# Kernel optimization log

Hardware: AMD Instinct MI355X
Metric: run time of the kernel (lower is better)

## Reference

```python
import jax, jax.numpy as jnp
import numpy as np

N_USERS = 100_000
N_ITEMS = 50_000
N = N_USERS + N_ITEMS
N_LAYERS = 3
ALPHA = 0.8
D = 64
IMG_D = 4096
TXT_D = 384
N_INTER = 2_000_000  # user-item interactions; symmetric nnz = 2*N_INTER


def setup_inputs() -> dict:
    # --- build symmetric-normalized bipartite adjacency (D^-1/2 A D^-1/2) in numpy ---
    rng = np.random.default_rng(0)
    u = rng.integers(0, N_USERS, N_INTER).astype(np.int32)
    i = (rng.integers(0, N_ITEMS, N_INTER) + N_USERS).astype(np.int32)
    rows = np.concatenate([u, i])
    cols = np.concatenate([i, u])
    deg = np.bincount(rows, minlength=N).astype(np.float32)
    d_inv = np.where(deg > 0, deg ** -0.5, 0.0).astype(np.float32)
    vals = d_inv[rows] * d_inv[cols]

    key = jax.random.key(0)
    ks = jax.random.split(key, 8)
    xav_img = float(np.sqrt(6.0 / (IMG_D + D)))
    xav_txt = float(np.sqrt(6.0 / (TXT_D + D)))
    return {
        "image_feats": jax.random.normal(ks[0], (N_ITEMS, IMG_D), jnp.float32),
        "text_feats": jax.random.normal(ks[1], (N_ITEMS, TXT_D), jnp.float32),
        "image_pref": jax.random.normal(ks[2], (N_USERS, D), jnp.float32),
        "text_pref": jax.random.normal(ks[3], (N_USERS, D), jnp.float32),
        "W_img": jax.random.uniform(ks[4], (IMG_D, D), jnp.float32, -xav_img, xav_img),
        "b_img": jnp.zeros((D,), jnp.float32),
        "W_txt": jax.random.uniform(ks[5], (TXT_D, D), jnp.float32, -xav_txt, xav_txt),
        "b_txt": jnp.zeros((D,), jnp.float32),
        "adj_vals": jnp.asarray(vals),
        "adj_rows": jnp.asarray(rows),
        "adj_cols": jnp.asarray(cols),
    }


def _spmm(rows, cols, vals, x):
    # sparse COO @ dense: out[r] += vals[e] * x[cols[e]]
    return jax.ops.segment_sum(vals[:, None] * x[cols], rows, num_segments=N)


def _l2norm(x):
    # F.normalize(x, dim=1): row-wise L2 with eps clamp
    return x / jnp.clip(jnp.linalg.norm(x, axis=1, keepdims=True), 1e-12)


def reference(image_feats, text_feats, image_pref, text_pref,
              W_img, b_img, W_txt, b_txt, adj_vals, adj_rows, adj_cols):
    img = _l2norm(image_feats @ W_img + b_img)   # [n_items, D]
    txt = _l2norm(text_feats @ W_txt + b_txt)    # [n_items, D]
    ego_i = jnp.concatenate([image_pref, img], axis=0)  # [N, D]
    ego_t = jnp.concatenate([text_pref, txt], axis=0)   # [N, D]
    for _ in range(N_LAYERS):
        ego_i = _spmm(adj_rows, adj_cols, adj_vals, ego_i) + ALPHA * ego_i
        ego_t = _spmm(adj_rows, adj_cols, adj_vals, ego_t) + ALPHA * ego_t
    user_preference = jnp.concatenate([ego_i[:N_USERS], ego_t[:N_USERS]], axis=1)  # [n_users, 2D]
    items = jnp.concatenate([ego_i[N_USERS:], ego_t[N_USERS:]], axis=1)            # [n_items, 2D]
    return user_preference, items
```

## Files before the change

### kernel.cpp

```cpp
#include <hip/hip_runtime.h>
#include <hip/hip_bf16.h>

#define N_USERS 100000
#define N_ITEMS 50000
#define N_TOTAL 150000
#define NNZ     4000000
#define ALPHA_F 0.8f
#define ELL_CAP 128

#define G_GEMM 782
#define G_COPY 512
#define G_SCAT 1024

typedef __attribute__((ext_vector_type(8))) short bf16x8;
typedef __attribute__((ext_vector_type(4))) float f32x4;

static __device__ __forceinline__ short f2bf(float f) {
    unsigned u = __builtin_bit_cast(unsigned, f);
    unsigned r = (u + 0x7fff + ((u >> 16) & 1)) >> 16;
    return (short)r;
}
static __device__ __forceinline__ unsigned pack_bf2(float a, float b) {
    return (unsigned)(unsigned short)f2bf(a) | ((unsigned)(unsigned short)f2bf(b) << 16);
}
static __device__ __forceinline__ float bf_lo(unsigned u) { return __uint_as_float(u << 16); }
static __device__ __forceinline__ float bf_hi(unsigned u) { return __uint_as_float(u & 0xFFFF0000u); }


__global__ __launch_bounds__(256) void prep_kernel(const float* __restrict__ Wimg,
                                                   const float* __restrict__ Wtxt,
                                                   int* __restrict__ cnt,
                                                   short* __restrict__ Wti,
                                                   short* __restrict__ Wtt) {
    const int T0 = N_TOTAL;
    const int T1 = T0 + 4096 * 64;
    const int T2 = T1 + 384 * 64;
    int i = blockIdx.x * 256 + threadIdx.x;
    int stride = gridDim.x * 256;
    for (; i < T2; i += stride) {
        if (i < T0) {
            cnt[i] = 0;
        } else if (i < T1) {
            int idx = i - T0; int k = idx >> 6, n = idx & 63;
            Wti[(size_t)n * 4096 + k] = f2bf(Wimg[(size_t)k * 64 + n]);
        } else {
            int idx = i - T1; int k = idx >> 6, n = idx & 63;
            Wtt[(size_t)n * 384 + k] = f2bf(Wtxt[(size_t)k * 64 + n]);
        }
    }
}


__global__ __launch_bounds__(256) void mega_kernel(
        const float* __restrict__ Aimg, const float* __restrict__ Atxt,
        const short* __restrict__ Wti, const short* __restrict__ Wtt,
        const float* __restrict__ bimg, const float* __restrict__ btxt,
        unsigned* __restrict__ egob,
        const int* __restrict__ rows, const int* __restrict__ cols,
        const float* __restrict__ vals, int* __restrict__ cnt, int2* __restrict__ ell,
        const float* __restrict__ img_pref, const float* __restrict__ txt_pref) {
    int b = blockIdx.x;
    if (b < G_GEMM) {
        const int M = N_ITEMS;
        int t = threadIdx.x;
        int wave = t >> 6, l = t & 63;
        int col = l & 15;
        int kb  = l >> 4;
        int row0 = b * 64 + wave * 16;
        int arow = row0 + col;
        bool rowok = arow < M;

        f32x4 ai0 = {0,0,0,0}, ai1 = ai0, ai2 = ai0, ai3 = ai0;
        f32x4 at0 = ai0, at1 = ai0, at2 = ai0, at3 = ai0;

        {
            const float* Ap = Aimg + (size_t)arow * 4096 + kb * 8;
            const short* Wp = Wti + (size_t)col * 4096 + kb * 8;
            for (int k0 = 0; k0 < 4096; k0 += 32) {
                float4 a0 = make_float4(0,0,0,0), a1 = a0;
                if (rowok) {
                    a0 = *reinterpret_cast<const float4*>(Ap + k0);
                    a1 = *reinterpret_cast<const float4*>(Ap + k0 + 4);
                }
                bf16x8 af;
                af[0]=f2bf(a0.x); af[1]=f2bf(a0.y); af[2]=f2bf(a0.z); af[3]=f2bf(a0.w);
                af[4]=f2bf(a1.x); af[5]=f2bf(a1.y); af[6]=f2bf(a1.z); af[7]=f2bf(a1.w);
                bf16x8 b0 = *reinterpret_cast<const bf16x8*>(Wp + k0);
                bf16x8 b1 = *reinterpret_cast<const bf16x8*>(Wp + (size_t)16 * 4096 + k0);
                bf16x8 b2 = *reinterpret_cast<const bf16x8*>(Wp + (size_t)32 * 4096 + k0);
                bf16x8 b3 = *reinterpret_cast<const bf16x8*>(Wp + (size_t)48 * 4096 + k0);
                ai0 = __builtin_amdgcn_mfma_f32_16x16x32_bf16(af, b0, ai0, 0, 0, 0);
                ai1 = __builtin_amdgcn_mfma_f32_16x16x32_bf16(af, b1, ai1, 0, 0, 0);
                ai2 = __builtin_amdgcn_mfma_f32_16x16x32_bf16(af, b2, ai2, 0, 0, 0);
                ai3 = __builtin_amdgcn_mfma_f32_16x16x32_bf16(af, b3, ai3, 0, 0, 0);
            }
        }
        {
            const float* Ap = Atxt + (size_t)arow * 384 + kb * 8;
            const short* Wp = Wtt + (size_t)col * 384 + kb * 8;
            for (int k0 = 0; k0 < 384; k0 += 32) {
                float4 a0 = make_float4(0,0,0,0), a1 = a0;
                if (rowok) {
                    a0 = *reinterpret_cast<const float4*>(Ap + k0);
                    a1 = *reinterpret_cast<const float4*>(Ap + k0 + 4);
                }
                bf16x8 af;
                af[0]=f2bf(a0.x); af[1]=f2bf(a0.y); af[2]=f2bf(a0.z); af[3]=f2bf(a0.w);
                af[4]=f2bf(a1.x); af[5]=f2bf(a1.y); af[6]=f2bf(a1.z); af[7]=f2bf(a1.w);
                bf16x8 b0 = *reinterpret_cast<const bf16x8*>(Wp + k0);
                bf16x8 b1 = *reinterpret_cast<const bf16x8*>(Wp + (size_t)16 * 384 + k0);
                bf16x8 b2 = *reinterpret_cast<const bf16x8*>(Wp + (size_t)32 * 384 + k0);
                bf16x8 b3 = *reinterpret_cast<const bf16x8*>(Wp + (size_t)48 * 384 + k0);
                at0 = __builtin_amdgcn_mfma_f32_16x16x32_bf16(af, b0, at0, 0, 0, 0);
                at1 = __builtin_amdgcn_mfma_f32_16x16x32_bf16(af, b1, at1, 0, 0, 0);
                at2 = __builtin_amdgcn_mfma_f32_16x16x32_bf16(af, b2, at2, 0, 0, 0);
                at3 = __builtin_amdgcn_mfma_f32_16x16x32_bf16(af, b3, at3, 0, 0, 0);
            }
        }

        float bi0 = bimg[ 0 + col], bi1 = bimg[16 + col], bi2 = bimg[32 + col], bi3 = bimg[48 + col];
        float bt0 = btxt[ 0 + col], bt1 = btxt[16 + col], bt2 = btxt[32 + col], bt3 = btxt[48 + col];
        #pragma unroll
        for (int i = 0; i < 4; ++i) {
            ai0[i] += bi0; ai1[i] += bi1; ai2[i] += bi2; ai3[i] += bi3;
            at0[i] += bt0; at1[i] += bt1; at2[i] += bt2; at3[i] += bt3;
        }
        unsigned* egob_items = egob + (size_t)N_USERS * 64;
        #pragma unroll
        for (int i = 0; i < 4; ++i) {
            float ssi = ai0[i]*ai0[i] + ai1[i]*ai1[i] + ai2[i]*ai2[i] + ai3[i]*ai3[i];
            float sst = at0[i]*at0[i] + at1[i]*at1[i] + at2[i]*at2[i] + at3[i]*at3[i];
            #pragma unroll
            for (int off = 1; off < 16; off <<= 1) {
                ssi += __shfl_xor(ssi, off, 64);
                sst += __shfl_xor(sst, off, 64);
            }
            float rni = 1.0f / fmaxf(sqrtf(ssi), 1e-12f);
            float rnt = 1.0f / fmaxf(sqrtf(sst), 1e-12f);
            int r = row0 + kb * 4 + i;
            if (r < M) {
                unsigned* ob = egob_items + (size_t)r * 64 + col;
                ob[ 0] = pack_bf2(ai0[i]*rni, at0[i]*rnt);
                ob[16] = pack_bf2(ai1[i]*rni, at1[i]*rnt);
                ob[32] = pack_bf2(ai2[i]*rni, at2[i]*rnt);
                ob[48] = pack_bf2(ai3[i]*rni, at3[i]*rnt);
            }
        }
    } else if (b < G_GEMM + G_COPY) {
        int idx = (b - G_GEMM) * 256 + threadIdx.x;
        int stride = G_COPY * 256;
        for (; idx < N_USERS * 16; idx += stride) {
            int row = idx >> 4, w4 = (idx & 15) << 2;
            float4 iv = *reinterpret_cast<const float4*>(&img_pref[(size_t)row * 64 + w4]);
            float4 tv = *reinterpret_cast<const float4*>(&txt_pref[(size_t)row * 64 + w4]);
            uint4 m;
            m.x = pack_bf2(iv.x, tv.x); m.y = pack_bf2(iv.y, tv.y);
            m.z = pack_bf2(iv.z, tv.z); m.w = pack_bf2(iv.w, tv.w);
            *reinterpret_cast<uint4*>(&egob[(size_t)row * 64 + w4]) = m;
        }
    } else {
        int i = (b - G_GEMM - G_COPY) * 256 + threadIdx.x;
        int stride = G_SCAT * 256;
        for (; i < NNZ; i += stride) {
            int r = rows[i];
            int p = atomicAdd(&cnt[r], 1);
            if (p < ELL_CAP)
                ell[(size_t)r * ELL_CAP + p] = make_int2(cols[i], __float_as_int(vals[i]));
        }
    }
}


__global__ __launch_bounds__(256) void sort_kernel(const int* __restrict__ cnt,
                                                   int2* __restrict__ ell) {
    int row = blockIdx.x * 4 + (threadIdx.x >> 6);
    if (row >= N_TOTAL) return;
    int lane = threadIdx.x & 63;
    int deg = min(cnt[row], ELL_CAP);
    if (deg <= 1) return;
    int2* base = ell + (size_t)row * ELL_CAP;
    int2 e0 = (lane < deg)      ? base[lane]      : make_int2(0x7FFFFFFF, 0);
    int2 e1 = (lane + 64 < deg) ? base[lane + 64] : make_int2(0x7FFFFFFF, 0);
    #pragma unroll
    for (int k = 2; k <= 128; k <<= 1) {
        #pragma unroll
        for (int j = 64; j >= 1; j >>= 1) {
            if (j >= k) continue;
            if (j == 64) {
                if (e0.x > e1.x) { int2 tmp = e0; e0 = e1; e1 = tmp; }
            } else {
                int2 p0, p1;
                p0.x = __shfl_xor(e0.x, j, 64); p0.y = __shfl_xor(e0.y, j, 64);
                p1.x = __shfl_xor(e1.x, j, 64); p1.y = __shfl_xor(e1.y, j, 64);
                bool up0 = ((lane & k) == 0);
                bool up1 = (((lane + 64) & k) == 0);
                bool lo0 = ((lane & j) == 0);
                bool lo1 = lo0;
                bool keepmin0 = (up0 == lo0);
                bool keepmin1 = (up1 == lo1);
                if (keepmin0 ? (e0.x > p0.x) : (e0.x < p0.x)) e0 = p0;
                if (keepmin1 ? (e1.x > p1.x) : (e1.x < p1.x)) e1 = p1;
            }
        }
    }
    if (lane < deg)      base[lane]      = e0;
    if (lane + 64 < deg) base[lane + 64] = e1;
}


__global__ __launch_bounds__(256) void spmm_kernel(
        const int* __restrict__ cnt, const int2* __restrict__ ell,
        const unsigned* __restrict__ xb,
        float* __restrict__ out32, unsigned* __restrict__ outb) {
    int row = blockIdx.x * 4 + (threadIdx.x >> 6);
    if (row >= N_TOTAL) return;
    int lane = threadIdx.x & 63;
    unsigned sw = xb[(size_t)row * 64 + lane];
    float2 acc;
    acc.x = ALPHA_F * bf_lo(sw);
    acc.y = ALPHA_F * bf_hi(sw);
    int deg = min(cnt[row], ELL_CAP);
    const int2* base = ell + (size_t)row * ELL_CAP;
    int i = 0;
    for (; i + 8 <= deg; i += 8) {
        int4 p0 = *reinterpret_cast<const int4*>(base + i);
        int4 p1 = *reinterpret_cast<const int4*>(base + i + 2);
        int4 p2 = *reinterpret_cast<const int4*>(base + i + 4);
        int4 p3 = *reinterpret_cast<const int4*>(base + i + 6);
        unsigned g0 = xb[(size_t)p0.x * 64 + lane];
        unsigned g1 = xb[(size_t)p0.z * 64 + lane];
        unsigned g2 = xb[(size_t)p1.x * 64 + lane];
        unsigned g3 = xb[(size_t)p1.z * 64 + lane];
        unsigned g4 = xb[(size_t)p2.x * 64 + lane];
        unsigned g5 = xb[(size_t)p2.z * 64 + lane];
        unsigned g6 = xb[(size_t)p3.x * 64 + lane];
        unsigned g7 = xb[(size_t)p3.z * 64 + lane];
        float v0 = __int_as_float(p0.y), v1 = __int_as_float(p0.w);
        float v2 = __int_as_float(p1.y), v3 = __int_as_float(p1.w);
        float v4 = __int_as_float(p2.y), v5 = __int_as_float(p2.w);
        float v6 = __int_as_float(p3.y), v7 = __int_as_float(p3.w);
        acc.x = fmaf(v0, bf_lo(g0), acc.x); acc.y = fmaf(v0, bf_hi(g0), acc.y);
        acc.x = fmaf(v1, bf_lo(g1), acc.x); acc.y = fmaf(v1, bf_hi(g1), acc.y);
        acc.x = fmaf(v2, bf_lo(g2), acc.x); acc.y = fmaf(v2, bf_hi(g2), acc.y);
        acc.x = fmaf(v3, bf_lo(g3), acc.x); acc.y = fmaf(v3, bf_hi(g3), acc.y);
        acc.x = fmaf(v4, bf_lo(g4), acc.x); acc.y = fmaf(v4, bf_hi(g4), acc.y);
        acc.x = fmaf(v5, bf_lo(g5), acc.x); acc.y = fmaf(v5, bf_hi(g5), acc.y);
        acc.x = fmaf(v6, bf_lo(g6), acc.x); acc.y = fmaf(v6, bf_hi(g6), acc.y);
        acc.x = fmaf(v7, bf_lo(g7), acc.x); acc.y = fmaf(v7, bf_hi(g7), acc.y);
    }
    for (; i < deg; ++i) {
        int2 c = base[i];
        float v = __int_as_float(c.y);
        unsigned g = xb[(size_t)c.x * 64 + lane];
        acc.x = fmaf(v, bf_lo(g), acc.x);
        acc.y = fmaf(v, bf_hi(g), acc.y);
    }
    if (out32) {
        out32[(size_t)row * 128 + lane] = acc.x;
        out32[(size_t)row * 128 + 64 + lane] = acc.y;
    }
    if (outb)
        outb[(size_t)row * 64 + lane] = pack_bf2(acc.x, acc.y);
}


extern "C" void kernel_launch(void* const* d_in, const int* in_sizes, int n_in,
                              void* d_out, int out_size, void* d_ws, size_t ws_size,
                              hipStream_t stream) {
    const float* image_feats = (const float*)d_in[0];
    const float* text_feats  = (const float*)d_in[1];
    const float* image_pref  = (const float*)d_in[2];
    const float* text_pref   = (const float*)d_in[3];
    const float* W_img       = (const float*)d_in[4];
    const float* b_img       = (const float*)d_in[5];
    const float* W_txt       = (const float*)d_in[6];
    const float* b_txt       = (const float*)d_in[7];
    const float* adj_vals    = (const float*)d_in[8];
    const int*   adj_rows    = (const int*)d_in[9];
    const int*   adj_cols    = (const int*)d_in[10];

    float* out = (float*)d_out;

    char* ws = (char*)d_ws;
    size_t off = 0;
    auto alloc = [&](size_t bytes) { char* p = ws + off; off += (bytes + 255) & ~size_t(255); return p; };
    int*      cnt    = (int*)     alloc(N_TOTAL * sizeof(int));
    int2*     ell    = (int2*)    alloc((size_t)N_TOTAL * ELL_CAP * sizeof(int2));
    unsigned* m0     = (unsigned*)alloc((size_t)N_TOTAL * 64 * sizeof(unsigned));
    unsigned* m1     = (unsigned*)alloc((size_t)N_TOTAL * 64 * sizeof(unsigned));
    short*    Wt_img = (short*)   alloc((size_t)64 * 4096 * sizeof(short));
    short*    Wt_txt = (short*)   alloc((size_t)64 * 384 * sizeof(short));
    (void)ws_size; (void)out_size; (void)n_in; (void)in_sizes;

    prep_kernel<<<512, 256, 0, stream>>>(W_img, W_txt, cnt, Wt_img, Wt_txt);

    mega_kernel<<<G_GEMM + G_COPY + G_SCAT, 256, 0, stream>>>(
        image_feats, text_feats, Wt_img, Wt_txt, b_img, b_txt, m0,
        adj_rows, adj_cols, adj_vals, cnt, ell, image_pref, text_pref);

    const int ROW_GRID = (N_TOTAL + 3) / 4;
    sort_kernel<<<ROW_GRID, 256, 0, stream>>>(cnt, ell);

    spmm_kernel<<<ROW_GRID, 256, 0, stream>>>(cnt, ell, m0, nullptr, m1);
    spmm_kernel<<<ROW_GRID, 256, 0, stream>>>(cnt, ell, m1, nullptr, m0);
    spmm_kernel<<<ROW_GRID, 256, 0, stream>>>(cnt, ell, m0, out, nullptr);
}
```

Measured before the change: 1.181 ms.

## Split GEMM into LDS double-buffered kernel with direct global-to-LDS loads

Moves the item projection GEMM out of the fused mega kernel into its own kernel. The new kernel stages A and W tiles into swizzled, double-buffered LDS with global_load_lds, so the next chunk loads while MFMA runs on the current one. This replaces the per-lane strided global loads of the old version. The scatter/copy work now runs as a separate kernel before the GEMM instead of concurrently in the same grid, which costs some overlap and adds a launch.

```diff
diff --git a/kernel.cpp b/kernel.cpp
--- a/kernel.cpp
+++ b/kernel.cpp
@@ -7,10 +7,10 @@
 #define NNZ     4000000
 #define ALPHA_F 0.8f
 #define ELL_CAP 128
-
-#define G_GEMM 782
-#define G_COPY 512
-#define G_SCAT 1024
+#define KCHUNK  128
+
+#define C_COPY 512
+#define C_SCAT 1024
 
 typedef __attribute__((ext_vector_type(8))) short bf16x8;
 typedef __attribute__((ext_vector_type(4))) float f32x4;
@@ -25,6 +25,12 @@
 }
 static __device__ __forceinline__ float bf_lo(unsigned u) { return __uint_as_float(u << 16); }
 static __device__ __forceinline__ float bf_hi(unsigned u) { return __uint_as_float(u & 0xFFFF0000u); }
+
+static __device__ __forceinline__ void gload_lds16(const void* src, void* dst) {
+    __builtin_amdgcn_global_load_lds(
+        (const __attribute__((address_space(1))) unsigned*)src,
+        (__attribute__((address_space(3))) unsigned*)dst, 16, 0, 0);
+}
 
 
 __global__ __launch_bounds__(256) void prep_kernel(const float* __restrict__ Wimg,
@@ -51,104 +57,15 @@
 }
 
 
-__global__ __launch_bounds__(256) void mega_kernel(
-        const float* __restrict__ Aimg, const float* __restrict__ Atxt,
-        const short* __restrict__ Wti, const short* __restrict__ Wtt,
-        const float* __restrict__ bimg, const float* __restrict__ btxt,
-        unsigned* __restrict__ egob,
+__global__ __launch_bounds__(256) void scat_copy_kernel(
         const int* __restrict__ rows, const int* __restrict__ cols,
         const float* __restrict__ vals, int* __restrict__ cnt, int2* __restrict__ ell,
-        const float* __restrict__ img_pref, const float* __restrict__ txt_pref) {
+        const float* __restrict__ img_pref, const float* __restrict__ txt_pref,
+        unsigned* __restrict__ egob) {
     int b = blockIdx.x;
-    if (b < G_GEMM) {
-        const int M = N_ITEMS;
-        int t = threadIdx.x;
-        int wave = t >> 6, l = t & 63;
-        int col = l & 15;
-        int kb  = l >> 4;
-        int row0 = b * 64 + wave * 16;
-        int arow = row0 + col;
-        bool rowok = arow < M;
-
-        f32x4 ai0 = {0,0,0,0}, ai1 = ai0, ai2 = ai0, ai3 = ai0;
-        f32x4 at0 = ai0, at1 = ai0, at2 = ai0, at3 = ai0;
-
-        {
-            const float* Ap = Aimg + (size_t)arow * 4096 + kb * 8;
-            const short* Wp = Wti + (size_t)col * 4096 + kb * 8;
-            for (int k0 = 0; k0 < 4096; k0 += 32) {
-                float4 a0 = make_float4(0,0,0,0), a1 = a0;
-                if (rowok) {
-                    a0 = *reinterpret_cast<const float4*>(Ap + k0);
-                    a1 = *reinterpret_cast<const float4*>(Ap + k0 + 4);
-                }
-                bf16x8 af;
-                af[0]=f2bf(a0.x); af[1]=f2bf(a0.y); af[2]=f2bf(a0.z); af[3]=f2bf(a0.w);
-                af[4]=f2bf(a1.x); af[5]=f2bf(a1.y); af[6]=f2bf(a1.z); af[7]=f2bf(a1.w);
-                bf16x8 b0 = *reinterpret_cast<const bf16x8*>(Wp + k0);
-                bf16x8 b1 = *reinterpret_cast<const bf16x8*>(Wp + (size_t)16 * 4096 + k0);
-                bf16x8 b2 = *reinterpret_cast<const bf16x8*>(Wp + (size_t)32 * 4096 + k0);
-                bf16x8 b3 = *reinterpret_cast<const bf16x8*>(Wp + (size_t)48 * 4096 + k0);
-                ai0 = __builtin_amdgcn_mfma_f32_16x16x32_bf16(af, b0, ai0, 0, 0, 0);
-                ai1 = __builtin_amdgcn_mfma_f32_16x16x32_bf16(af, b1, ai1, 0, 0, 0);
-                ai2 = __builtin_amdgcn_mfma_f32_16x16x32_bf16(af, b2, ai2, 0, 0, 0);
-                ai3 = __builtin_amdgcn_mfma_f32_16x16x32_bf16(af, b3, ai3, 0, 0, 0);
-            }
-        }
-        {
-            const float* Ap = Atxt + (size_t)arow * 384 + kb * 8;
-            const short* Wp = Wtt + (size_t)col * 384 + kb * 8;
-            for (int k0 = 0; k0 < 384; k0 += 32) {
-                float4 a0 = make_float4(0,0,0,0), a1 = a0;
-                if (rowok) {
-                    a0 = *reinterpret_cast<const float4*>(Ap + k0);
-                    a1 = *reinterpret_cast<const float4*>(Ap + k0 + 4);
-                }
-                bf16x8 af;
-                af[0]=f2bf(a0.x); af[1]=f2bf(a0.y); af[2]=f2bf(a0.z); af[3]=f2bf(a0.w);
-                af[4]=f2bf(a1.x); af[5]=f2bf(a1.y); af[6]=f2bf(a1.z); af[7]=f2bf(a1.w);
-                bf16x8 b0 = *reinterpret_cast<const bf16x8*>(Wp + k0);
-                bf16x8 b1 = *reinterpret_cast<const bf16x8*>(Wp + (size_t)16 * 384 + k0);
-                bf16x8 b2 = *reinterpret_cast<const bf16x8*>(Wp + (size_t)32 * 384 + k0);
-                bf16x8 b3 = *reinterpret_cast<const bf16x8*>(Wp + (size_t)48 * 384 + k0);
-                at0 = __builtin_amdgcn_mfma_f32_16x16x32_bf16(af, b0, at0, 0, 0, 0);
-                at1 = __builtin_amdgcn_mfma_f32_16x16x32_bf16(af, b1, at1, 0, 0, 0);
-                at2 = __builtin_amdgcn_mfma_f32_16x16x32_bf16(af, b2, at2, 0, 0, 0);
-                at3 = __builtin_amdgcn_mfma_f32_16x16x32_bf16(af, b3, at3, 0, 0, 0);
-            }
-        }
-
-        float bi0 = bimg[ 0 + col], bi1 = bimg[16 + col], bi2 = bimg[32 + col], bi3 = bimg[48 + col];
-        float bt0 = btxt[ 0 + col], bt1 = btxt[16 + col], bt2 = btxt[32 + col], bt3 = btxt[48 + col];
-        #pragma unroll
-        for (int i = 0; i < 4; ++i) {
-            ai0[i] += bi0; ai1[i] += bi1; ai2[i] += bi2; ai3[i] += bi3;
-            at0[i] += bt0; at1[i] += bt1; at2[i] += bt2; at3[i] += bt3;
-        }
-        unsigned* egob_items = egob + (size_t)N_USERS * 64;
-        #pragma unroll
-        for (int i = 0; i < 4; ++i) {
-            float ssi = ai0[i]*ai0[i] + ai1[i]*ai1[i] + ai2[i]*ai2[i] + ai3[i]*ai3[i];
-            float sst = at0[i]*at0[i] + at1[i]*at1[i] + at2[i]*at2[i] + at3[i]*at3[i];
-            #pragma unroll
-            for (int off = 1; off < 16; off <<= 1) {
-                ssi += __shfl_xor(ssi, off, 64);
-                sst += __shfl_xor(sst, off, 64);
-            }
-            float rni = 1.0f / fmaxf(sqrtf(ssi), 1e-12f);
-            float rnt = 1.0f / fmaxf(sqrtf(sst), 1e-12f);
-            int r = row0 + kb * 4 + i;
-            if (r < M) {
-                unsigned* ob = egob_items + (size_t)r * 64 + col;
-                ob[ 0] = pack_bf2(ai0[i]*rni, at0[i]*rnt);
-                ob[16] = pack_bf2(ai1[i]*rni, at1[i]*rnt);
-                ob[32] = pack_bf2(ai2[i]*rni, at2[i]*rnt);
-                ob[48] = pack_bf2(ai3[i]*rni, at3[i]*rnt);
-            }
-        }
-    } else if (b < G_GEMM + G_COPY) {
-        int idx = (b - G_GEMM) * 256 + threadIdx.x;
-        int stride = G_COPY * 256;
+    if (b < C_COPY) {
+        int idx = b * 256 + threadIdx.x;
+        int stride = C_COPY * 256;
         for (; idx < N_USERS * 16; idx += stride) {
             int row = idx >> 4, w4 = (idx & 15) << 2;
             float4 iv = *reinterpret_cast<const float4*>(&img_pref[(size_t)row * 64 + w4]);
@@ -159,13 +76,143 @@
             *reinterpret_cast<uint4*>(&egob[(size_t)row * 64 + w4]) = m;
         }
     } else {
-        int i = (b - G_GEMM - G_COPY) * 256 + threadIdx.x;
-        int stride = G_SCAT * 256;
+        int i = (b - C_COPY) * 256 + threadIdx.x;
+        int stride = C_SCAT * 256;
         for (; i < NNZ; i += stride) {
             int r = rows[i];
             int p = atomicAdd(&cnt[r], 1);
             if (p < ELL_CAP)
                 ell[(size_t)r * ELL_CAP + p] = make_int2(cols[i], __float_as_int(vals[i]));
+        }
+    }
+}
+
+
+static __device__ __forceinline__ void compute_chunk(
+        const float* at, const short* bt, int wave, int lane,
+        f32x4& c0, f32x4& c1, f32x4& c2, f32x4& c3) {
+    const int col = lane & 15, kb = lane >> 4;
+    const int arow = 16 * wave + col;
+    const int aswz = (col & 7) << 4;
+    const int bswz = col << 4;
+    const char* abase = (const char*)at + arow * 512;
+    const char* bbase = (const char*)bt + col * 256;
+    #pragma unroll
+    for (int ks = 0; ks < 4; ++ks) {
+        int Xa = ks * 128 + kb * 32;
+        float4 a0v = *(const float4*)(abase + ((Xa)      ^ aswz));
+        float4 a1v = *(const float4*)(abase + ((Xa + 16) ^ aswz));
+        bf16x8 af;
+        af[0]=f2bf(a0v.x); af[1]=f2bf(a0v.y); af[2]=f2bf(a0v.z); af[3]=f2bf(a0v.w);
+        af[4]=f2bf(a1v.x); af[5]=f2bf(a1v.y); af[6]=f2bf(a1v.z); af[7]=f2bf(a1v.w);
+        int xb = (ks * 64 + kb * 16) ^ bswz;
+        bf16x8 b0 = *(const bf16x8*)(bbase + xb);
+        bf16x8 b1 = *(const bf16x8*)(bbase + 16 * 256 + xb);
+        bf16x8 b2 = *(const bf16x8*)(bbase + 32 * 256 + xb);
+        bf16x8 b3 = *(const bf16x8*)(bbase + 48 * 256 + xb);
+        c0 = __builtin_amdgcn_mfma_f32_16x16x32_bf16(af, b0, c0, 0, 0, 0);
+        c1 = __builtin_amdgcn_mfma_f32_16x16x32_bf16(af, b1, c1, 0, 0, 0);
+        c2 = __builtin_amdgcn_mfma_f32_16x16x32_bf16(af, b2, c2, 0, 0, 0);
+        c3 = __builtin_amdgcn_mfma_f32_16x16x32_bf16(af, b3, c3, 0, 0, 0);
+    }
+}
+
+__global__ __launch_bounds__(256) void gemm_lds_kernel(
+        const float* __restrict__ Aimg, const float* __restrict__ Atxt,
+        const short* __restrict__ Wti, const short* __restrict__ Wtt,
+        const float* __restrict__ bimg, const float* __restrict__ btxt,
+        unsigned* __restrict__ egob_items) {
+    __shared__ __align__(16) float atile[2][64 * KCHUNK];
+    __shared__ __align__(16) short btile[2][64 * KCHUNK];
+    const int t = threadIdx.x;
+    const int wave = t >> 6, lane = t & 63;
+    const int col = lane & 15, kb = lane >> 4;
+    const int row0 = blockIdx.x * 64;
+    const int gmax = N_ITEMS - 1;
+
+    const int s_arow  = 16 * wave + (lane >> 5);
+    const int s_axoff = (lane & 31) * 16;
+    const int s_bcol  = 16 * wave + (lane >> 4);
+    const int s_bxoff = (lane & 15) * 16;
+
+    auto stageA = [&](const float* A, int K, int k0, int bi) {
+        #pragma unroll
+        for (int c = 0; c < 8; ++c) {
+            int r = s_arow + 2 * c;
+            int gr = row0 + r; gr = gr > gmax ? gmax : gr;
+            int sw = (r & 7) << 4;
+            const char* src = (const char*)A + ((size_t)gr * K + k0) * 4 + (s_axoff ^ sw);
+            char* dst = (char*)&atile[bi][0] + r * 512 + s_axoff;
+            gload_lds16(src, dst);
+        }
+    };
+    auto stageB = [&](const short* W, int K, int k0, int bi) {
+        #pragma unroll
+        for (int c = 0; c < 4; ++c) {
+            int bc = s_bcol + 4 * c;
+            int sw = (bc & 15) << 4;
+            const char* src = (const char*)W + ((size_t)bc * K + k0) * 2 + (s_bxoff ^ sw);
+            char* dst = (char*)&btile[bi][0] + bc * 256 + s_bxoff;
+            gload_lds16(src, dst);
+        }
+    };
+
+    f32x4 z = {0.f, 0.f, 0.f, 0.f};
+    f32x4 ai0 = z, ai1 = z, ai2 = z, ai3 = z;
+    f32x4 at0 = z, at1 = z, at2 = z, at3 = z;
+
+    stageA(Aimg, 4096, 0, 0); stageB(Wti, 4096, 0, 0);
+    asm volatile("s_waitcnt vmcnt(0)" ::: "memory");
+    __syncthreads();
+    for (int ch = 0; ch < 32; ++ch) {
+        int bi = ch & 1;
+        if (ch + 1 < 32) {
+            stageA(Aimg, 4096, (ch + 1) * KCHUNK, bi ^ 1);
+            stageB(Wti, 4096, (ch + 1) * KCHUNK, bi ^ 1);
+        }
+        compute_chunk(&atile[bi][0], &btile[bi][0], wave, lane, ai0, ai1, ai2, ai3);
+        asm volatile("s_waitcnt vmcnt(0)" ::: "memory");
+        __syncthreads();
+    }
+    stageA(Atxt, 384, 0, 0); stageB(Wtt, 384, 0, 0);
+    asm volatile("s_waitcnt vmcnt(0)" ::: "memory");
+    __syncthreads();
+    for (int ch = 0; ch < 3; ++ch) {
+        int bi = ch & 1;
+        if (ch + 1 < 3) {
+            stageA(Atxt, 384, (ch + 1) * KCHUNK, bi ^ 1);
+            stageB(Wtt, 384, (ch + 1) * KCHUNK, bi ^ 1);
+        }
+        compute_chunk(&atile[bi][0], &btile[bi][0], wave, lane, at0, at1, at2, at3);
+        asm volatile("s_waitcnt vmcnt(0)" ::: "memory");
+        __syncthreads();
+    }
+
+    float bi0 = bimg[ 0 + col], bi1 = bimg[16 + col], bi2 = bimg[32 + col], bi3 = bimg[48 + col];
+    float bt0 = btxt[ 0 + col], bt1 = btxt[16 + col], bt2 = btxt[32 + col], bt3 = btxt[48 + col];
+    #pragma unroll
+    for (int i = 0; i < 4; ++i) {
+        ai0[i] += bi0; ai1[i] += bi1; ai2[i] += bi2; ai3[i] += bi3;
+        at0[i] += bt0; at1[i] += bt1; at2[i] += bt2; at3[i] += bt3;
+    }
+    #pragma unroll
+    for (int i = 0; i < 4; ++i) {
+        float ssi = ai0[i]*ai0[i] + ai1[i]*ai1[i] + ai2[i]*ai2[i] + ai3[i]*ai3[i];
+        float sst = at0[i]*at0[i] + at1[i]*at1[i] + at2[i]*at2[i] + at3[i]*at3[i];
+        #pragma unroll
+        for (int off = 1; off < 16; off <<= 1) {
+            ssi += __shfl_xor(ssi, off, 64);
+            sst += __shfl_xor(sst, off, 64);
+        }
+        float rni = 1.0f / fmaxf(sqrtf(ssi), 1e-12f);
+        float rnt = 1.0f / fmaxf(sqrtf(sst), 1e-12f);
+        int r = row0 + 16 * wave + kb * 4 + i;
+        if (r < N_ITEMS) {
+            unsigned* ob = egob_items + (size_t)r * 64 + col;
+            ob[ 0] = pack_bf2(ai0[i]*rni, at0[i]*rnt);
+            ob[16] = pack_bf2(ai1[i]*rni, at1[i]*rnt);
+            ob[32] = pack_bf2(ai2[i]*rni, at2[i]*rnt);
+            ob[48] = pack_bf2(ai3[i]*rni, at3[i]*rnt);
         }
     }
 }
@@ -195,9 +242,8 @@
                 bool up0 = ((lane & k) == 0);
                 bool up1 = (((lane + 64) & k) == 0);
                 bool lo0 = ((lane & j) == 0);
-                bool lo1 = lo0;
                 bool keepmin0 = (up0 == lo0);
-                bool keepmin1 = (up1 == lo1);
+                bool keepmin1 = (up1 == lo0);
                 if (keepmin0 ? (e0.x > p0.x) : (e0.x < p0.x)) e0 = p0;
                 if (keepmin1 ? (e1.x > p1.x) : (e1.x < p1.x)) e1 = p1;
             }
@@ -294,9 +340,12 @@
 
     prep_kernel<<<512, 256, 0, stream>>>(W_img, W_txt, cnt, Wt_img, Wt_txt);
 
-    mega_kernel<<<G_GEMM + G_COPY + G_SCAT, 256, 0, stream>>>(
-        image_feats, text_feats, Wt_img, Wt_txt, b_img, b_txt, m0,
-        adj_rows, adj_cols, adj_vals, cnt, ell, image_pref, text_pref);
+    scat_copy_kernel<<<C_COPY + C_SCAT, 256, 0, stream>>>(
+        adj_rows, adj_cols, adj_vals, cnt, ell, image_pref, text_pref, m0);
+
+    unsigned* m0_items = m0 + (size_t)N_USERS * 64;
+    gemm_lds_kernel<<<(N_ITEMS + 63) / 64, 256, 0, stream>>>(
+        image_feats, text_feats, Wt_img, Wt_txt, b_img, b_txt, m0_items);
 
     const int ROW_GRID = (N_TOTAL + 3) / 4;
     sort_kernel<<<ROW_GRID, 256, 0, stream>>>(cnt, ell);
```

Measured after the change: 1.141 ms. -3.4%, faster.
